# Optimization experiments

Measured on AMD Instinct MI355X. Metric: run time of the kernel, lower is better.

Reference implementation:

```python
import jax, jax.numpy as jnp
import numpy as np

N_NODES = 100000
N_EDGES = 1600000
IN_FEAT = 512
HIDDEN = 128
N_CLASSES = 7


def gcn_conv(x, edge_index, edge_weight, W, b):
    """PyG GCNConv: add self-loops (weight 1), symmetric normalization, linear, scatter-add, bias."""
    n = x.shape[0]
    src = jnp.concatenate([edge_index[0], jnp.arange(n, dtype=edge_index.dtype)])
    dst = jnp.concatenate([edge_index[1], jnp.arange(n, dtype=edge_index.dtype)])
    w = jnp.concatenate([edge_weight, jnp.ones((n,), dtype=edge_weight.dtype)])
    deg = jax.ops.segment_sum(w, dst, num_segments=n)  # degree on destination (col)
    dinv = jnp.where(deg > 0, jax.lax.rsqrt(deg), 0.0)
    norm = dinv[src] * w * dinv[dst]                   # [E+N]
    h = x @ W                                          # [N, out] transform BEFORE propagate
    msg = h[src] * norm[:, None]                       # [E+N, out] irregular gather
    out = jax.ops.segment_sum(msg, dst, num_segments=n)  # scatter-reduce
    return out + b


def setup_inputs() -> dict:
    key = jax.random.key(0)
    k1, k2, k3, k4, k5, k6 = jax.random.split(key, 6)
    x = jax.random.normal(k1, (N_NODES, IN_FEAT), dtype=jnp.float32)
    edge_index = jax.random.randint(k2, (2, N_EDGES), 0, N_NODES, dtype=jnp.int32)
    edge_weight = jax.random.uniform(k3, (N_EDGES,), dtype=jnp.float32)
    s1 = 1.0 / np.sqrt(IN_FEAT)
    s2 = 1.0 / np.sqrt(HIDDEN)
    W1 = jax.random.uniform(k4, (IN_FEAT, HIDDEN), dtype=jnp.float32, minval=-s1, maxval=s1)
    b1 = jnp.zeros((HIDDEN,), dtype=jnp.float32)
    W2 = jax.random.uniform(k5, (HIDDEN, N_CLASSES), dtype=jnp.float32, minval=-s2, maxval=s2)
    b2 = jnp.zeros((N_CLASSES,), dtype=jnp.float32)
    return {"x": x, "edge_index": edge_index, "edge_weight": edge_weight,
            "W1": W1, "b1": b1, "W2": W2, "b2": b2}


def reference(x, edge_index, edge_weight, W1, b1, W2, b2):
    # eval mode: F.dropout(training=False) is identity
    h = jax.nn.elu(gcn_conv(x, edge_index, edge_weight, W1, b1))
    out = gcn_conv(h, edge_index, edge_weight, W2, b2)
    return jax.nn.log_softmax(out, axis=1)
```

## Files before the change

kernel.cpp:

```cpp
#include <hip/hip_runtime.h>
#include <math.h>

#define N_NODES 100000
#define N_EDGES 1600000
#define IN_F 512
#define HID 128
#define NCLS 7

#define DEG_SHIFT 43
#define DEG_WMASK ((1ull << 43) - 1)
#define DEG_SCALE 4194304.0f
#define DEG_INV_SCALE (1.0f / 4194304.0f)
#define NB_SCAN 98

#define FILL_BLOCKS 3125
#define GEMM_BLOCKS 782
#define G2 (FILL_BLOCKS + GEMM_BLOCKS)

typedef short short8 __attribute__((ext_vector_type(8)));
typedef float f32x4 __attribute__((ext_vector_type(4)));
typedef unsigned long long u64;

__device__ __forceinline__ unsigned pack_bf16x2(float a, float b) {
  unsigned ua = __float_as_uint(a), ub = __float_as_uint(b);
  unsigned ra = (ua + 0x7FFFu + ((ua >> 16) & 1u)) >> 16;
  unsigned rb = (ub + 0x7FFFu + ((ub >> 16) & 1u)) >> 16;
  return ra | (rb << 16);
}
__device__ __forceinline__ unsigned short f32_to_bf16(float v) {
  unsigned u = __float_as_uint(v);
  return (unsigned short)((u + 0x7FFFu + ((u >> 16) & 1u)) >> 16);
}
__device__ __forceinline__ float bf_lo(unsigned u) { return __uint_as_float(u << 16); }
__device__ __forceinline__ float bf_hi(unsigned u) { return __uint_as_float(u & 0xFFFF0000u); }

__global__ void k_deg(const int* __restrict__ ei, const float* __restrict__ ew,
                      unsigned long long* __restrict__ packed, int* __restrict__ rank) {
  int e = blockIdx.x * 256 + threadIdx.x;
  int d = ei[N_EDGES + e];
  u64 fx = (u64)(ew[e] * DEG_SCALE + 0.5f);
  u64 old = atomicAdd(&packed[d], (1ull << DEG_SHIFT) | fx);
  rank[e] = (int)(old >> DEG_SHIFT);
}

__global__ void k_mid(const unsigned long long* __restrict__ packed,
                      float* __restrict__ dinv, int* __restrict__ cnt, int* __restrict__ bsum,
                      const float* __restrict__ W1, uint4* __restrict__ w1bf,
                      uint2* __restrict__ csr_pad) {
  const int b = blockIdx.x, t = threadIdx.x;
  if (b >= NB_SCAN) {
    int idx = (b - NB_SCAN) * 256 + t;
    if (idx < 8) csr_pad[idx] = make_uint2(0u, 0u);
    int lane = idx & 63;
    int st = idx >> 6;
    int tt = st & 7, ss = st >> 3;
    int n = tt * 16 + (lane & 15);
    int k0 = ss * 32 + (lane >> 4) * 8;
    uint4 v;
    v.x = pack_bf16x2(W1[(size_t)(k0 + 0) * HID + n], W1[(size_t)(k0 + 1) * HID + n]);
    v.y = pack_bf16x2(W1[(size_t)(k0 + 2) * HID + n], W1[(size_t)(k0 + 3) * HID + n]);
    v.z = pack_bf16x2(W1[(size_t)(k0 + 4) * HID + n], W1[(size_t)(k0 + 5) * HID + n]);
    v.w = pack_bf16x2(W1[(size_t)(k0 + 6) * HID + n], W1[(size_t)(k0 + 7) * HID + n]);
    w1bf[idx] = v;
    return;
  }
  __shared__ int sh[256];
  int base = b * 1024;
  int v = 0;
#pragma unroll
  for (int q = 0; q < 4; q++) {
    int idx = base + t * 4 + q;
    if (idx < N_NODES) {
      unsigned long long p = packed[idx];
      int c = (int)(p >> DEG_SHIFT);
      cnt[idx] = c;
      dinv[idx] = rsqrtf((float)(p & DEG_WMASK) * DEG_INV_SCALE + 1.0f);
      v += c;
    }
  }
  sh[t] = v;
  __syncthreads();
  for (int o = 128; o > 0; o >>= 1) {
    if (t < o) sh[t] += sh[t + o];
    __syncthreads();
  }
  if (t == 0) bsum[b] = sh[0];
}

__global__ void k_scan_final(const int* __restrict__ cnt, const int* __restrict__ bsum,
                             int* __restrict__ offs) {
  __shared__ int s[256];
  int t = threadIdx.x;
  int c = (t < NB_SCAN && t < blockIdx.x) ? bsum[t] : 0;
  s[t] = c;
  __syncthreads();
  for (int o = 128; o > 0; o >>= 1) {
    if (t < o) s[t] += s[t + o];
    __syncthreads();
  }
  int block_off = s[0];
  __syncthreads();
  int base = blockIdx.x * 1024;
  int v[4]; int sum = 0;
#pragma unroll
  for (int q = 0; q < 4; q++) {
    int idx = base + t * 4 + q;
    v[q] = (idx < N_NODES) ? cnt[idx] : 0;
    sum += v[q];
  }
  s[t] = sum;
  __syncthreads();
  for (int o = 1; o < 256; o <<= 1) {
    int x = (t >= o) ? s[t - o] : 0;
    __syncthreads();
    s[t] += x;
    __syncthreads();
  }
  int acc = s[t] - sum + block_off;
#pragma unroll
  for (int q = 0; q < 4; q++) {
    int idx = base + t * 4 + q;
    if (idx < N_NODES) offs[idx] = acc;
    acc += v[q];
  }
}

__global__ __launch_bounds__(512) void k_fillgemm(
    const int* __restrict__ ei, const float* __restrict__ ew,
    const int* __restrict__ rank, const int* __restrict__ offs, uint2* __restrict__ csr,
    const float* __restrict__ x, const uint4* __restrict__ w1bf,
    const float* __restrict__ dinv, unsigned short* __restrict__ h_u16) {
  __shared__ uint4 lds_b[2048];
  const int bx = blockIdx.x;
  const int tid = threadIdx.x;

  if (bx % 5 != 0) {
    int fb = bx - bx / 5 - 1;
    int e = fb * 512 + tid;
    int s = ei[e];
    int d = ei[N_EDGES + e];
    int p = offs[d] + rank[e];
    csr[p] = make_uint2((unsigned)s, __float_as_uint(ew[e]));
    return;
  }

  const int gb = bx / 5;
  const int lane = tid & 63;
  const int wv = tid >> 6;
  const int gw = gb * 8 + wv;
  const int m0 = gw * 16;
  const bool act = (m0 < N_NODES);
  const int l16 = lane & 15, quad = lane >> 4;
  const float* arow = x + (size_t)(m0 + l16) * IN_F + quad * 8;

  f32x4 acc[8];
#pragma unroll
  for (int t = 0; t < 8; t++) acc[t] = (f32x4){0.f, 0.f, 0.f, 0.f};

  for (int q = 0; q < 4; q++) {
    float4 v[8];
    if (act) {
#pragma unroll
      for (int ks = 0; ks < 4; ks++) {
        const float* ap = arow + q * 128 + ks * 32;
        v[2 * ks]     = *(const float4*)ap;
        v[2 * ks + 1] = *(const float4*)(ap + 4);
      }
    }
    if (q > 0) __syncthreads();
#pragma unroll
    for (int j = 0; j < 4; j++)
      lds_b[tid + j * 512] = w1bf[q * 2048 + tid + j * 512];
    __syncthreads();
    if (act) {
#pragma unroll
      for (int ks = 0; ks < 4; ks++) {
        uint4 au;
        au.x = pack_bf16x2(v[2 * ks].x, v[2 * ks].y);
        au.y = pack_bf16x2(v[2 * ks].z, v[2 * ks].w);
        au.z = pack_bf16x2(v[2 * ks + 1].x, v[2 * ks + 1].y);
        au.w = pack_bf16x2(v[2 * ks + 1].z, v[2 * ks + 1].w);
        short8 af = *(short8*)&au;
        const uint4* bbase = lds_b + ks * 512 + lane;
#pragma unroll
        for (int t = 0; t < 8; t++) {
          uint4 bv = bbase[t * 64];
          acc[t] = __builtin_amdgcn_mfma_f32_16x16x32_bf16(af, *(const short8*)&bv,
                                                           acc[t], 0, 0, 0);
        }
      }
    }
  }
  if (act) {
    float df[4];
#pragma unroll
    for (int r = 0; r < 4; r++) df[r] = dinv[m0 + quad * 4 + r];
#pragma unroll
    for (int t = 0; t < 8; t++)
#pragma unroll
      for (int r = 0; r < 4; r++)
        h_u16[(size_t)(m0 + quad * 4 + r) * HID + t * 16 + l16] = f32_to_bf16(acc[t][r] * df[r]);
  }
}

__global__ __launch_bounds__(256) void k_agg1(const unsigned* __restrict__ h_u,
    const float* __restrict__ dinv, const int* __restrict__ offs, const int* __restrict__ cnt,
    const uint2* __restrict__ csr, const float* __restrict__ b1,
    const float* __restrict__ W2, float* __restrict__ h2) {
  int i = blockIdx.x * 4 + (threadIdx.x >> 6);
  int lane = threadIdx.x & 63;
  if (i >= N_NODES) return;
  float w2a[NCLS], w2b[NCLS];
#pragma unroll
  for (int c = 0; c < NCLS; c++) {
    w2a[c] = W2[(size_t)(2 * lane) * NCLS + c];
    w2b[c] = W2[(size_t)(2 * lane + 1) * NCLS + c];
  }
  int start = offs[i], len = cnt[i];
  int end = start + len;
  float ax = 0.f, ay = 0.f;
  for (int p = start; p < end; p += 8) {
    uint2 e[8];
#pragma unroll
    for (int k = 0; k < 8; k++) e[k] = csr[p + k];
    unsigned u[8];
#pragma unroll
    for (int k = 0; k < 8; k++) u[k] = h_u[(size_t)e[k].x * 64 + lane];
#pragma unroll
    for (int k = 0; k < 8; k++) {
      float n = (k == 0 || p + k < end) ? __uint_as_float(e[k].y) : 0.f;
      ax = fmaf(bf_lo(u[k]), n, ax);
      ay = fmaf(bf_hi(u[k]), n, ay);
    }
  }
  float di = dinv[i];
  unsigned u = h_u[(size_t)i * 64 + lane];
  float2 bb = *(const float2*)(b1 + lane * 2);
  float vx = fmaf(di, ax + bf_lo(u), bb.x);
  float vy = fmaf(di, ay + bf_hi(u), bb.y);
  vx = vx > 0.f ? vx : expm1f(vx);
  vy = vy > 0.f ? vy : expm1f(vy);
  float s[NCLS];
#pragma unroll
  for (int c = 0; c < NCLS; c++) s[c] = fmaf(vy, w2b[c], vx * w2a[c]);
#pragma unroll
  for (int m = 1; m < 64; m <<= 1) {
#pragma unroll
    for (int c = 0; c < NCLS; c++) s[c] += __shfl_xor(s[c], m);
  }
  if (lane < 8) {
    float v = lane == 0 ? s[0] : lane == 1 ? s[1] : lane == 2 ? s[2] :
              lane == 3 ? s[3] : lane == 4 ? s[4] : lane == 5 ? s[5] : s[6];
    h2[(size_t)i * 8 + lane] = (lane < NCLS) ? v * di : 0.f;
  }
}

__global__ __launch_bounds__(256) void k_agg2(const float* __restrict__ h2,
    const float* __restrict__ dinv, const int* __restrict__ offs, const int* __restrict__ cnt,
    const uint2* __restrict__ csr, const float* __restrict__ b2, float* __restrict__ out) {
  int tid = threadIdx.x;
  int i = blockIdx.x * 32 + (tid >> 3);
  int f = tid & 7;
  if (i >= N_NODES) return;
  int start = offs[i], len = cnt[i];
  int end = start + len;
  float acc = 0.0f;
  for (int p = start; p < end; p += 4) {
    uint2 e0 = csr[p];
    uint2 e1 = csr[p + 1];
    uint2 e2 = csr[p + 2];
    uint2 e3 = csr[p + 3];
    float v0 = h2[(size_t)e0.x * 8 + f];
    float v1 = h2[(size_t)e1.x * 8 + f];
    float v2 = h2[(size_t)e2.x * 8 + f];
    float v3 = h2[(size_t)e3.x * 8 + f];
    float n0 = __uint_as_float(e0.y);
    float n1 = (p + 1 < end) ? __uint_as_float(e1.y) : 0.f;
    float n2 = (p + 2 < end) ? __uint_as_float(e2.y) : 0.f;
    float n3 = (p + 3 < end) ? __uint_as_float(e3.y) : 0.f;
    acc = fmaf(v0, n0, acc);
    acc = fmaf(v1, n1, acc);
    acc = fmaf(v2, n2, acc);
    acc = fmaf(v3, n3, acc);
  }
  float di = dinv[i];
  float v = fmaf(di, acc + h2[(size_t)i * 8 + f], (f < NCLS) ? b2[f] : 0.0f);
  float vm = (f < NCLS) ? v : -INFINITY;
#pragma unroll
  for (int o = 1; o < 8; o <<= 1) vm = fmaxf(vm, __shfl_xor(vm, o, 8));
  float ex = (f < NCLS) ? expf(v - vm) : 0.0f;
  float s8 = ex;
#pragma unroll
  for (int o = 1; o < 8; o <<= 1) s8 += __shfl_xor(s8, o, 8);
  float lse = logf(s8);
  if (f < NCLS) out[(size_t)i * NCLS + f] = v - vm - lse;
}

extern "C" void kernel_launch(void* const* d_in, const int* in_sizes, int n_in,
                              void* d_out, int out_size, void* d_ws, size_t ws_size,
                              hipStream_t stream) {
  const float* x  = (const float*)d_in[0];
  const int*   ei = (const int*)d_in[1];
  const float* ew = (const float*)d_in[2];
  const float* W1 = (const float*)d_in[3];
  const float* b1 = (const float*)d_in[4];
  const float* W2 = (const float*)d_in[5];
  const float* b2 = (const float*)d_in[6];
  float* out = (float*)d_out;

  char* w = (char*)d_ws;
  const size_t Npad  = ((size_t)N_NODES * 4 + 255) & ~(size_t)255;
  const size_t Npad8 = ((size_t)N_NODES * 8 + 255) & ~(size_t)255;
  const size_t Epad  = ((size_t)N_EDGES * 4 + 255) & ~(size_t)255;
  size_t off = 0;
  unsigned long long* packed = (unsigned long long*)(w + off); off += Npad8;
  float*    dinv     = (float*)(w + off);    off += Npad;
  int*      cnt      = (int*)(w + off);      off += Npad;
  int*      offs     = (int*)(w + off);      off += Npad;
  int*      bsum     = (int*)(w + off);      off += 1024;
  int*      rank     = (int*)(w + off);      off += Epad;
  uint2*    csr      = (uint2*)(w + off);    off += ((size_t)(N_EDGES + 8) * 8 + 255) & ~(size_t)255;
  uint4*    w1bf     = (uint4*)(w + off);    off += (size_t)8192 * 16;
  unsigned short* h_u16 = (unsigned short*)(w + off); off += (size_t)N_NODES * HID * 2;
  float*    h2       = (float*)(w + off);    off += (size_t)N_NODES * 8 * 4;

  hipMemsetAsync(packed, 0, Npad8, stream);

  k_deg<<<N_EDGES / 256, 256, 0, stream>>>(ei, ew, packed, rank);
  k_mid<<<NB_SCAN + 32, 256, 0, stream>>>(packed, dinv, cnt, bsum, W1, w1bf, csr + N_EDGES);
  k_scan_final<<<NB_SCAN, 256, 0, stream>>>(cnt, bsum, offs);
  k_fillgemm<<<G2, 512, 0, stream>>>(ei, ew, rank, offs, csr, x, w1bf, dinv, h_u16);
  k_agg1<<<(N_NODES + 3) / 4, 256, 0, stream>>>((const unsigned*)h_u16, dinv, offs, cnt,
                                                csr, b1, W2, h2);
  k_agg2<<<N_NODES / 32, 256, 0, stream>>>(h2, dinv, offs, cnt, csr, b2, out);
}
```

Before: 494.8 us.

## Pre-convert x to bf16 fragment layout inside the degree kernel

Merges the fp32-to-bf16 conversion of x into the degree-counting kernel, interleaving conversion blocks with atomic degree blocks. The result is stored in an MFMA-fragment-ordered bf16 buffer. The GEMM then loads all of a wave's A fragments up front as bf16, with no per-iteration conversion. The aim is to hide the conversion behind the atomic-bound degree pass and halve the GEMM's read bytes. The cost is an extra write and read of a roughly 100 MB intermediate buffer.

```diff
diff --git a/kernel.cpp b/kernel.cpp
--- a/kernel.cpp
+++ b/kernel.cpp
@@ -13,6 +13,7 @@
 #define DEG_INV_SCALE (1.0f / 4194304.0f)
 #define NB_SCAN 98
 
+#define G_DEGCONV 31250
 #define FILL_BLOCKS 3125
 #define GEMM_BLOCKS 782
 #define G2 (FILL_BLOCKS + GEMM_BLOCKS)
@@ -34,13 +35,35 @@
 __device__ __forceinline__ float bf_lo(unsigned u) { return __uint_as_float(u << 16); }
 __device__ __forceinline__ float bf_hi(unsigned u) { return __uint_as_float(u & 0xFFFF0000u); }
 
-__global__ void k_deg(const int* __restrict__ ei, const float* __restrict__ ew,
-                      unsigned long long* __restrict__ packed, int* __restrict__ rank) {
-  int e = blockIdx.x * 256 + threadIdx.x;
-  int d = ei[N_EDGES + e];
-  u64 fx = (u64)(ew[e] * DEG_SCALE + 0.5f);
-  u64 old = atomicAdd(&packed[d], (1ull << DEG_SHIFT) | fx);
-  rank[e] = (int)(old >> DEG_SHIFT);
+__global__ void k_degconv(const int* __restrict__ ei, const float* __restrict__ ew,
+                          unsigned long long* __restrict__ packed, int* __restrict__ rank,
+                          const float* __restrict__ x, uint4* __restrict__ xbf) {
+  const int bx = blockIdx.x, tid = threadIdx.x;
+  if (bx % 5 == 0) {
+    int e = (bx / 5) * 256 + tid;
+    int d = ei[N_EDGES + e];
+    u64 fx = (u64)(ew[e] * DEG_SCALE + 0.5f);
+    u64 old = atomicAdd(&packed[d], (1ull << DEG_SHIFT) | fx);
+    rank[e] = (int)(old >> DEG_SHIFT);
+    return;
+  }
+  int cb = bx - bx / 5 - 1;
+  int chunk = cb * 256 + tid;
+  int gw = chunk >> 10;
+  int rem = chunk & 1023;
+  int ks2 = rem >> 6;
+  int lane = rem & 63;
+  int m = gw * 16 + (lane & 15);
+  int kbase = ks2 * 32 + (lane >> 4) * 8;
+  const float* ap = x + (size_t)m * IN_F + kbase;
+  float4 a0 = *(const float4*)ap;
+  float4 a1 = *(const float4*)(ap + 4);
+  uint4 v;
+  v.x = pack_bf16x2(a0.x, a0.y);
+  v.y = pack_bf16x2(a0.z, a0.w);
+  v.z = pack_bf16x2(a1.x, a1.y);
+  v.w = pack_bf16x2(a1.z, a1.w);
+  xbf[chunk] = v;
 }
 
 __global__ void k_mid(const unsigned long long* __restrict__ packed,
@@ -128,7 +151,7 @@
 __global__ __launch_bounds__(512) void k_fillgemm(
     const int* __restrict__ ei, const float* __restrict__ ew,
     const int* __restrict__ rank, const int* __restrict__ offs, uint2* __restrict__ csr,
-    const float* __restrict__ x, const uint4* __restrict__ w1bf,
+    const uint4* __restrict__ xbf, const uint4* __restrict__ w1bf,
     const float* __restrict__ dinv, unsigned short* __restrict__ h_u16) {
   __shared__ uint4 lds_b[2048];
   const int bx = blockIdx.x;
@@ -151,22 +174,19 @@
   const int m0 = gw * 16;
   const bool act = (m0 < N_NODES);
   const int l16 = lane & 15, quad = lane >> 4;
-  const float* arow = x + (size_t)(m0 + l16) * IN_F + quad * 8;
+
+  uint4 a[16];
+  if (act) {
+    const uint4* ab = xbf + (size_t)gw * 1024 + lane;
+#pragma unroll
+    for (int i = 0; i < 16; i++) a[i] = ab[i * 64];
+  }
 
   f32x4 acc[8];
 #pragma unroll
   for (int t = 0; t < 8; t++) acc[t] = (f32x4){0.f, 0.f, 0.f, 0.f};
 
   for (int q = 0; q < 4; q++) {
-    float4 v[8];
-    if (act) {
-#pragma unroll
-      for (int ks = 0; ks < 4; ks++) {
-        const float* ap = arow + q * 128 + ks * 32;
-        v[2 * ks]     = *(const float4*)ap;
-        v[2 * ks + 1] = *(const float4*)(ap + 4);
-      }
-    }
     if (q > 0) __syncthreads();
 #pragma unroll
     for (int j = 0; j < 4; j++)
@@ -175,12 +195,7 @@
     if (act) {
 #pragma unroll
       for (int ks = 0; ks < 4; ks++) {
-        uint4 au;
-        au.x = pack_bf16x2(v[2 * ks].x, v[2 * ks].y);
-        au.y = pack_bf16x2(v[2 * ks].z, v[2 * ks].w);
-        au.z = pack_bf16x2(v[2 * ks + 1].x, v[2 * ks + 1].y);
-        au.w = pack_bf16x2(v[2 * ks + 1].z, v[2 * ks + 1].w);
-        short8 af = *(short8*)&au;
+        short8 af = *(const short8*)&a[q * 4 + ks];
         const uint4* bbase = lds_b + ks * 512 + lane;
 #pragma unroll
         for (int t = 0; t < 8; t++) {
@@ -321,15 +336,16 @@
   int*      rank     = (int*)(w + off);      off += Epad;
   uint2*    csr      = (uint2*)(w + off);    off += ((size_t)(N_EDGES + 8) * 8 + 255) & ~(size_t)255;
   uint4*    w1bf     = (uint4*)(w + off);    off += (size_t)8192 * 16;
+  uint4*    xbf      = (uint4*)(w + off);    off += (size_t)6256 * 1024 * 16;
   unsigned short* h_u16 = (unsigned short*)(w + off); off += (size_t)N_NODES * HID * 2;
   float*    h2       = (float*)(w + off);    off += (size_t)N_NODES * 8 * 4;
 
   hipMemsetAsync(packed, 0, Npad8, stream);
 
-  k_deg<<<N_EDGES / 256, 256, 0, stream>>>(ei, ew, packed, rank);
+  k_degconv<<<G_DEGCONV, 256, 0, stream>>>(ei, ew, packed, rank, x, xbf);
   k_mid<<<NB_SCAN + 32, 256, 0, stream>>>(packed, dinv, cnt, bsum, W1, w1bf, csr + N_EDGES);
   k_scan_final<<<NB_SCAN, 256, 0, stream>>>(cnt, bsum, offs);
-  k_fillgemm<<<G2, 512, 0, stream>>>(ei, ew, rank, offs, csr, x, w1bf, dinv, h_u16);
+  k_fillgemm<<<G2, 512, 0, stream>>>(ei, ew, rank, offs, csr, xbf, w1bf, dinv, h_u16);
   k_agg1<<<(N_NODES + 3) / 4, 256, 0, stream>>>((const unsigned*)h_u16, dinv, offs, cnt,
                                                 csr, b1, W2, h2);
   k_agg2<<<N_NODES / 32, 256, 0, stream>>>(h2, dinv, offs, cnt, csr, b2, out);
```

New measurement: 482.9 us. 1.02x faster.
